# Optimization experiments

Hardware: AMD Instinct MI355X
Metric: run time of the kernel (lower is better)

Reference implementation:

```python
import jax, jax.numpy as jnp
import numpy as np

B, S, D = 1, 2048, 512
H, KH, DH = 8, 2, 64
G = H // KH            # grouped queries per kv head
CBS = SBS = 32         # compress / selection block size (equal)
NSEL = 8               # num selected blocks
WIN = 128              # sliding window size
NC = S // CBS          # num compressed blocks
NF = S // SBS          # num fine blocks (S divisible by SBS)
CDIM = CBS * DH


def setup_inputs():
    key = jax.random.key(0)
    ks = jax.random.split(key, 12)
    r = lambda k, shape, s=0.02: jax.random.normal(k, shape, dtype=jnp.float32) * s
    return {
        "inp": jax.random.normal(ks[0], (B, S, D), dtype=jnp.float32),
        "norm_w": jnp.ones((D,), jnp.float32),
        "w_qkv": r(ks[1], (D, H * DH + 2 * KH * DH)),
        "mem_kv": r(ks[2], (2, KH, 1, DH)),
        "k_pos": r(ks[3], (KH, CBS, DH)),
        "v_pos": r(ks[4], (KH, CBS, DH)),
        "kc_w1": r(ks[5], (CDIM, CDIM)), "kc_b1": jnp.zeros((CDIM,), jnp.float32),
        "kc_w2": r(ks[6], (CDIM, DH)), "kc_b2": jnp.zeros((DH,), jnp.float32),
        "vc_w1": r(ks[7], (CDIM, CDIM)), "vc_b1": jnp.zeros((CDIM,), jnp.float32),
        "vc_w2": r(ks[8], (CDIM, DH)), "vc_b2": jnp.zeros((DH,), jnp.float32),
        "comb_w": r(ks[9], (D, 3 * H)),
        "comb_b": jnp.tile(jnp.array([-2.0, -2.0, 2.0], jnp.float32), H),
        "out_w": r(ks[10], (H * DH, D)),
    }


def _rope(x):  # x: [b, h, n, d]; interleaved rotary (rotary-embedding-torch style)
    d, n = x.shape[-1], x.shape[-2]
    inv = 1.0 / (10000.0 ** (jnp.arange(0, d, 2, dtype=jnp.float32) / d))
    fr = jnp.arange(n, dtype=jnp.float32)[:, None] * inv[None, :]  # [n, d/2]
    fr = jnp.repeat(fr, 2, axis=-1)                                 # [n, d]
    cos, sin = jnp.cos(fr), jnp.sin(fr)
    xp = x.reshape(*x.shape[:-1], d // 2, 2)
    xr = jnp.stack((-xp[..., 1], xp[..., 0]), axis=-1).reshape(x.shape)
    return x * cos + xr * sin


def _mlp(x, w1, b1, w2, b2):
    return jax.nn.relu(x @ w1 + b1) @ w2 + b2


def _forward(inp, norm_w, w_qkv, mem_kv, k_pos, v_pos, kc_w1, kc_b1, kc_w2, kc_b2,
             vc_w1, vc_b1, vc_w2, vc_b2, comb_w, comb_b, out_w):
    scale = DH ** -0.5
    NEG = -jnp.finfo(jnp.float32).max

    # RMSNorm
    x = inp * jax.lax.rsqrt(jnp.mean(inp * inp, -1, keepdims=True)
                            + jnp.finfo(jnp.float32).eps) * norm_w

    qkv = x @ w_qkv
    q, k, v = jnp.split(qkv, [H * DH, H * DH + KH * DH], axis=-1)
    q = q.reshape(B, S, H, DH).transpose(0, 2, 1, 3)    # b h n d
    k = k.reshape(B, S, KH, DH).transpose(0, 2, 1, 3)   # b kh n d
    v = v.reshape(B, S, KH, DH).transpose(0, 2, 1, 3)

    # --- 1. compressed attention (unrotated q/k) ---
    kb = k.reshape(B, KH, NC, CBS, DH) + k_pos[None, :, None]
    vb = v.reshape(B, KH, NC, CBS, DH) + v_pos[None, :, None]
    ck = _mlp(kb.reshape(B, KH, NC, CDIM), kc_w1, kc_b1, kc_w2, kc_b2)  # b kh nc d
    cv = _mlp(vb.reshape(B, KH, NC, CDIM), vc_w1, vc_b1, vc_w2, vc_b2)
    ck = jnp.concatenate((jnp.broadcast_to(mem_kv[0][None], (B, KH, 1, DH)), ck), axis=2)
    cv = jnp.concatenate((jnp.broadcast_to(mem_kv[1][None], (B, KH, 1, DH)), cv), axis=2)

    ck_pos = jnp.concatenate((jnp.array([-1]), (jnp.arange(NC) + 1) * CBS - 1))
    cmask = ck_pos[None, :] < jnp.arange(S)[:, None]     # [S, 1+NC]

    qg = q.reshape(B, KH, G, S, DH)
    csim = jnp.einsum('bhgid,bhjd->bhgij', qg, ck) * scale
    csim = jnp.where(cmask, csim, NEG)
    cattn = jax.nn.softmax(csim, axis=-1)
    c_out = jnp.einsum('bhgij,bhjd->bhgid', cattn, cv)   # b kh g n d

    # --- importance scores -> top-k block selection (shared across grouped queries) ---
    imp = csim[..., 1:].mean(axis=2)                     # b kh n nc
    imp = jnp.pad(imp, ((0, 0), (0, 0), (0, 0), (1, 0)), constant_values=-1e3)
    imp = jax.nn.softmax(imp, axis=-1)[..., 1:]
    sel_val, sel_idx = jax.lax.top_k(imp, NSEL)          # b kh n sel

    # --- rotary for fine + sliding branches ---
    qr, kr = _rope(q), _rope(k)

    # --- 2. fine (selected-block) attention ---
    own = jnp.broadcast_to((jnp.arange(S) // SBS)[None, None, :, None], (B, KH, S, 1))
    sel_idx = jnp.concatenate((sel_idx, own), axis=-1)   # b kh n (sel+1), own block appended

    bmask = jnp.broadcast_to((sel_val > 1e-10)[..., None], (B, KH, S, NSEL, SBS))
    tri = jnp.tril(jnp.ones((SBS, SBS), bool))
    diag = jnp.broadcast_to(jnp.tile(tri, (NF, 1))[None, None, :, None, :], (B, KH, S, 1, SBS))
    fmask = jnp.concatenate((bmask, diag), axis=-2).reshape(B, KH, 1, S, (NSEL + 1) * SBS)

    kfb = kr.reshape(B, KH, NF, SBS, DH)
    vfb = v.reshape(B, KH, NF, SBS, DH)
    gidx = sel_idx[..., None, None]                      # b kh n sel1 1 1
    fk = jnp.take_along_axis(kfb[:, :, None], gidx, axis=3).reshape(B, KH, S, (NSEL + 1) * SBS, DH)
    fv = jnp.take_along_axis(vfb[:, :, None], gidx, axis=3).reshape(B, KH, S, (NSEL + 1) * SBS, DH)

    fqg = qr.reshape(B, KH, G, S, DH)
    fsim = jnp.einsum('bhgid,bhijd->bhgij', fqg, fk) * scale
    fsim = jnp.where(fmask, fsim, NEG)
    fattn = jax.nn.softmax(fsim, axis=-1)
    f_out = jnp.einsum('bhgij,bhijd->bhgid', fattn, fv)  # b kh g n d

    diff = jnp.arange(S)[:, None] - jnp.arange(S)[None, :]
    smask = (diff >= 0) & (diff <= WIN)
    ssim = jnp.einsum('bhgid,bhjd->bhgij', fqg, kr) * scale
    ssim = jnp.where(smask, ssim, NEG)
    sattn = jax.nn.softmax(ssim, axis=-1)
    s_out = jnp.einsum('bhgij,bhjd->bhgid', sattn, v)    # b kh g n d

    # --- learned gating combine over [compressed, fine, sliding] ---
    gates = jax.nn.sigmoid(x @ comb_w + comb_b).reshape(B, S, H, 3)
    gates = gates.transpose(0, 2, 1, 3).reshape(B, KH, G, S, 3)
    out = gates[..., 0:1] * c_out + gates[..., 1:2] * f_out + gates[..., 2:3] * s_out
    out = out.reshape(B, H, S, DH).transpose(0, 2, 1, 3).reshape(B, S, H * DH)
    return out @ out_w


def reference(inp, norm_w, w_qkv, mem_kv, k_pos, v_pos, kc_w1, kc_b1, kc_w2, kc_b2,
              vc_w1, vc_b1, vc_w2, vc_b2, comb_w, comb_b, out_w):
    return _forward(inp, norm_w, w_qkv, mem_kv, k_pos, v_pos, kc_w1, kc_b1, kc_w2, kc_b2,
                    vc_w1, vc_b1, vc_w2, vc_b2, comb_w, comb_b, out_w)
```

## Files before the change

kernel.cpp:

```cpp
#include <hip/hip_runtime.h>
#include <hip/hip_bf16.h>
#include <math.h>

#define S 2048
#define D 512
#define H 8
#define KH 2
#define DH 64
#define G 4
#define CBS 32
#define NSEL 8
#define WIN 128
#define NC 64
#define CDIM 2048

typedef __attribute__((ext_vector_type(8))) short bf16x8_t;
typedef __attribute__((ext_vector_type(4))) float f32x4_t;
typedef __attribute__((ext_vector_type(2))) _Float16 half2v;

static __device__ __forceinline__ unsigned short f2bf(float f) {
    union { float f; unsigned int u; } v; v.f = f;
    unsigned int r = (v.u + 0x7FFFu + ((v.u >> 16) & 1u)) >> 16;
    return (unsigned short)r;
}
static __device__ __forceinline__ float bf2f(unsigned short h) {
    union { unsigned int u; float f; } v; v.u = ((unsigned int)h) << 16;
    return v.f;
}
static __device__ __forceinline__ float bflo(unsigned int u) {
    union { unsigned int u; float f; } v; v.u = u << 16; return v.f;
}
static __device__ __forceinline__ float bfhi(unsigned int u) {
    union { unsigned int u; float f; } v; v.u = u & 0xffff0000u; return v.f;
}
static __device__ __forceinline__ unsigned short f2h(float f) {
    union { _Float16 h; unsigned short s; } v; v.h = (_Float16)f; return v.s;
}
static __device__ __forceinline__ float h2f(unsigned short u) {
    union { unsigned short s; _Float16 h; } v; v.s = u; return (float)v.h;
}
static __device__ __forceinline__ float dot2f16(unsigned int a, unsigned int b, float c) {
    union { unsigned int u; half2v h; } A, B; A.u = a; B.u = b;
    return __builtin_amdgcn_fdot2(A.h, B.h, c, false);
}

__global__ __launch_bounds__(256) void k_rmsnorm(const float* __restrict__ inp,
                                                 const float* __restrict__ w,
                                                 unsigned short* __restrict__ xbf) {
    int s = blockIdx.x; int t = threadIdx.x;
    const float* row = inp + (size_t)s * D;
    float a = row[t], b = row[t + 256];
    float ss = a * a + b * b;
    for (int off = 32; off; off >>= 1) ss += __shfl_xor(ss, off);
    __shared__ float red[4];
    if ((t & 63) == 0) red[t >> 6] = ss;
    __syncthreads();
    float tot = red[0] + red[1] + red[2] + red[3];
    float inv = rsqrtf(tot / (float)D + 1.1920929e-07f);
    xbf[(size_t)s * D + t]       = f2bf(a * inv * w[t]);
    xbf[(size_t)s * D + t + 256] = f2bf(b * inv * w[t + 256]);
}

__global__ void k_rope_table(float* __restrict__ ct, float* __restrict__ st) {
    int idx = blockIdx.x * 256 + threadIdx.x;
    int s = idx >> 5, p = idx & 31;
    float inv = powf(10000.0f, -(float)p / 32.0f);
    float fr = (float)s * inv;
    ct[idx] = cosf(fr); st[idx] = sinf(fr);
}

__global__ __launch_bounds__(256) void k_gemm0(
    const unsigned short* __restrict__ A,
    const float* __restrict__ W,
    const float* __restrict__ k_pos, const float* __restrict__ v_pos,
    const float* __restrict__ ct, const float* __restrict__ st,
    float* __restrict__ qb,
    unsigned short* __restrict__ qr16, unsigned short* __restrict__ kr16,
    unsigned short* __restrict__ v16, unsigned short* __restrict__ kbvb)
{
    const int K = 512, N = 768;
    __shared__ __align__(16) unsigned short As[64][40];
    __shared__ __align__(16) unsigned short Bs[64][40];
    int t = threadIdx.x;
    int m0 = blockIdx.y * 64, n0 = blockIdx.x * 64;
    int wave = t >> 6, lane = t & 63;
    int mh = wave & 1, nh = wave >> 1;
    f32x4_t acc[2][2] = {};
    int ar = t >> 2, ac = (t & 3) * 8;
    int bk = t >> 3, bn = (t & 7) * 8;
    int arow_l = lane & 15, kcol = (lane >> 4) * 8;
    uint4 aReg = *(const uint4*)&A[(size_t)(m0 + ar) * K + ac];
    const float4* wr = (const float4*)&W[(size_t)bk * N + n0 + bn];
    float4 w0 = wr[0], w1 = wr[1];
    for (int k0 = 0; k0 < K; k0 += 32) {
        __syncthreads();
        *(uint4*)&As[ar][ac] = aReg;
        unsigned short bp[8];
        bp[0] = f2bf(w0.x); bp[1] = f2bf(w0.y); bp[2] = f2bf(w0.z); bp[3] = f2bf(w0.w);
        bp[4] = f2bf(w1.x); bp[5] = f2bf(w1.y); bp[6] = f2bf(w1.z); bp[7] = f2bf(w1.w);
        #pragma unroll
        for (int j = 0; j < 8; ++j) Bs[bn + j][bk] = bp[j];
        __syncthreads();
        if (k0 + 32 < K) {
            aReg = *(const uint4*)&A[(size_t)(m0 + ar) * K + k0 + 32 + ac];
            wr = (const float4*)&W[(size_t)(k0 + 32 + bk) * N + n0 + bn];
            w0 = wr[0]; w1 = wr[1];
        }
        bf16x8_t a0 = *(const bf16x8_t*)&As[mh * 32 + arow_l][kcol];
        bf16x8_t a1 = *(const bf16x8_t*)&As[mh * 32 + 16 + arow_l][kcol];
        bf16x8_t b0v = *(const bf16x8_t*)&Bs[nh * 32 + arow_l][kcol];
        bf16x8_t b1v = *(const bf16x8_t*)&Bs[nh * 32 + 16 + arow_l][kcol];
        acc[0][0] = __builtin_amdgcn_mfma_f32_16x16x32_bf16(a0, b0v, acc[0][0], 0, 0, 0);
        acc[0][1] = __builtin_amdgcn_mfma_f32_16x16x32_bf16(a0, b1v, acc[0][1], 0, 0, 0);
        acc[1][0] = __builtin_amdgcn_mfma_f32_16x16x32_bf16(a1, b0v, acc[1][0], 0, 0, 0);
        acc[1][1] = __builtin_amdgcn_mfma_f32_16x16x32_bf16(a1, b1v, acc[1][1], 0, 0, 0);
    }
    #pragma unroll
    for (int mi = 0; mi < 2; ++mi)
    #pragma unroll
    for (int ni = 0; ni < 2; ++ni)
    #pragma unroll
    for (int r = 0; r < 4; ++r) {
        int gm = m0 + mh * 32 + mi * 16 + (lane >> 4) * 4 + r;
        int gn = n0 + nh * 32 + ni * 16 + (lane & 15);
        float val = acc[mi][ni][r];
        float part = __shfl_xor(val, 1);
        if (gn < 512) {
            int hh = gn >> 6, d = gn & 63;
            size_t idx = ((size_t)hh * S + gm) * DH + d;
            qb[idx] = val;
            int p = d >> 1;
            float cc = ct[gm * 32 + p], sn = st[gm * 32 + p];
            float y = (d & 1) ? (val * cc + part * sn) : (val * cc - part * sn);
            qr16[idx] = f2h(y);
        } else if (gn < 640) {
            int gk = gn - 512, khh = gk >> 6, d = gk & 63;
            size_t idx = ((size_t)khh * S + gm) * DH + d;
            int p = d >> 1;
            float cc = ct[gm * 32 + p], sn = st[gm * 32 + p];
            float y = (d & 1) ? (val * cc + part * sn) : (val * cc - part * sn);
            kr16[idx] = f2h(y);
            int tt = gm & 31, nc2 = gm >> 5;
            kbvb[((size_t)(khh * 64 + nc2)) * 2048 + tt * 64 + d] =
                f2bf(val + k_pos[(khh * CBS + tt) * 64 + d]);
        } else {
            int gv = gn - 640, khh = gv >> 6, d = gv & 63;
            size_t idx = ((size_t)khh * S + gm) * DH + d;
            v16[idx] = f2bf(val);
            int tt = gm & 31, nc2 = gm >> 5;
            kbvb[((size_t)(128 + khh * 64 + nc2)) * 2048 + tt * 64 + d] =
                f2bf(val + v_pos[(khh * CBS + tt) * 64 + d]);
        }
    }
}

template<int MODE>
__global__ __launch_bounds__(256) void k_gemm(
    const unsigned short* __restrict__ A,
    const float* __restrict__ B0,
    const float* __restrict__ B1,
    const float* __restrict__ bias0, const float* __restrict__ bias1,
    int M, int N, int K,
    unsigned short* __restrict__ hid, float* __restrict__ outC)
{
    __shared__ __align__(16) unsigned short As[64][40];
    __shared__ __align__(16) unsigned short Bs[64][40];
    int t = threadIdx.x;
    int m0 = blockIdx.y * 64, n0 = blockIdx.x * 64;
    const float* W = B0;
    const float* bias = bias0;
    if (MODE == 1 && blockIdx.y >= 2) { W = B1; bias = bias1; }
    int wave = t >> 6, lane = t & 63;
    int mh = wave & 1, nh = wave >> 1;
    f32x4_t acc[2][2] = {};
    int ar = t >> 2, ac = (t & 3) * 8;
    int bk = t >> 3, bn = (t & 7) * 8;
    int arow_l = lane & 15, kcol = (lane >> 4) * 8;
    uint4 aReg = *(const uint4*)&A[(size_t)(m0 + ar) * K + ac];
    const float4* wr = (const float4*)&W[(size_t)bk * N + n0 + bn];
    float4 w0 = wr[0], w1 = wr[1];
    for (int k0 = 0; k0 < K; k0 += 32) {
        __syncthreads();
        *(uint4*)&As[ar][ac] = aReg;
        unsigned short bp[8];
        bp[0] = f2bf(w0.x); bp[1] = f2bf(w0.y); bp[2] = f2bf(w0.z); bp[3] = f2bf(w0.w);
        bp[4] = f2bf(w1.x); bp[5] = f2bf(w1.y); bp[6] = f2bf(w1.z); bp[7] = f2bf(w1.w);
        #pragma unroll
        for (int j = 0; j < 8; ++j) Bs[bn + j][bk] = bp[j];
        __syncthreads();
        if (k0 + 32 < K) {
            aReg = *(const uint4*)&A[(size_t)(m0 + ar) * K + k0 + 32 + ac];
            wr = (const float4*)&W[(size_t)(k0 + 32 + bk) * N + n0 + bn];
            w0 = wr[0]; w1 = wr[1];
        }
        bf16x8_t a0 = *(const bf16x8_t*)&As[mh * 32 + arow_l][kcol];
        bf16x8_t a1 = *(const bf16x8_t*)&As[mh * 32 + 16 + arow_l][kcol];
        bf16x8_t b0v = *(const bf16x8_t*)&Bs[nh * 32 + arow_l][kcol];
        bf16x8_t b1v = *(const bf16x8_t*)&Bs[nh * 32 + 16 + arow_l][kcol];
        acc[0][0] = __builtin_amdgcn_mfma_f32_16x16x32_bf16(a0, b0v, acc[0][0], 0, 0, 0);
        acc[0][1] = __builtin_amdgcn_mfma_f32_16x16x32_bf16(a0, b1v, acc[0][1], 0, 0, 0);
        acc[1][0] = __builtin_amdgcn_mfma_f32_16x16x32_bf16(a1, b0v, acc[1][0], 0, 0, 0);
        acc[1][1] = __builtin_amdgcn_mfma_f32_16x16x32_bf16(a1, b1v, acc[1][1], 0, 0, 0);
    }
    #pragma unroll
    for (int mi = 0; mi < 2; ++mi)
    #pragma unroll
    for (int ni = 0; ni < 2; ++ni)
    #pragma unroll
    for (int r = 0; r < 4; ++r) {
        int gm = m0 + mh * 32 + mi * 16 + (lane >> 4) * 4 + r;
        int gn = n0 + nh * 32 + ni * 16 + (lane & 15);
        float val = acc[mi][ni][r];
        if (MODE == 1) {
            float h = val + bias[gn]; if (h < 0.f) h = 0.f;
            hid[(size_t)gm * N + gn] = f2bf(h);
        } else {
            outC[(size_t)gm * N + gn] = val;
        }
    }
}

__global__ __launch_bounds__(256) void k_mlp2p(
    const unsigned short* __restrict__ A,
    const float* __restrict__ kc_w2, const float* __restrict__ vc_w2,
    float* __restrict__ part)
{
    const int N = 64, LDA = 2048;
    __shared__ __align__(16) unsigned short As[64][40];
    __shared__ __align__(16) unsigned short Bs[64][40];
    int t = threadIdx.x;
    int ks = blockIdx.x, m0 = blockIdx.y * 64;
    int kbeg = ks * 512;
    const float* W = (blockIdx.y >= 2) ? vc_w2 : kc_w2;
    int wave = t >> 6, lane = t & 63;
    int mh = wave & 1, nh = wave >> 1;
    f32x4_t acc[2][2] = {};
    int ar = t >> 2, ac = (t & 3) * 8;
    int bk = t >> 3, bn = (t & 7) * 8;
    int arow_l = lane & 15, kcol = (lane >> 4) * 8;
    uint4 aReg = *(const uint4*)&A[(size_t)(m0 + ar) * LDA + kbeg + ac];
    const float4* wr = (const float4*)&W[(size_t)(kbeg + bk) * N + bn];
    float4 w0 = wr[0], w1 = wr[1];
    for (int k0 = 0; k0 < 512; k0 += 32) {
        __syncthreads();
        *(uint4*)&As[ar][ac] = aReg;
        unsigned short bp[8];
        bp[0] = f2bf(w0.x); bp[1] = f2bf(w0.y); bp[2] = f2bf(w0.z); bp[3] = f2bf(w0.w);
        bp[4] = f2bf(w1.x); bp[5] = f2bf(w1.y); bp[6] = f2bf(w1.z); bp[7] = f2bf(w1.w);
        #pragma unroll
        for (int j = 0; j < 8; ++j) Bs[bn + j][bk] = bp[j];
        __syncthreads();
        if (k0 + 32 < 512) {
            aReg = *(const uint4*)&A[(size_t)(m0 + ar) * LDA + kbeg + k0 + 32 + ac];
            wr = (const float4*)&W[(size_t)(kbeg + k0 + 32 + bk) * N + bn];
            w0 = wr[0]; w1 = wr[1];
        }
        bf16x8_t a0 = *(const bf16x8_t*)&As[mh * 32 + arow_l][kcol];
        bf16x8_t a1 = *(const bf16x8_t*)&As[mh * 32 + 16 + arow_l][kcol];
        bf16x8_t b0v = *(const bf16x8_t*)&Bs[nh * 32 + arow_l][kcol];
        bf16x8_t b1v = *(const bf16x8_t*)&Bs[nh * 32 + 16 + arow_l][kcol];
        acc[0][0] = __builtin_amdgcn_mfma_f32_16x16x32_bf16(a0, b0v, acc[0][0], 0, 0, 0);
        acc[0][1] = __builtin_amdgcn_mfma_f32_16x16x32_bf16(a0, b1v, acc[0][1], 0, 0, 0);
        acc[1][0] = __builtin_amdgcn_mfma_f32_16x16x32_bf16(a1, b0v, acc[1][0], 0, 0, 0);
        acc[1][1] = __builtin_amdgcn_mfma_f32_16x16x32_bf16(a1, b1v, acc[1][1], 0, 0, 0);
    }
    #pragma unroll
    for (int mi = 0; mi < 2; ++mi)
    #pragma unroll
    for (int ni = 0; ni < 2; ++ni)
    #pragma unroll
    for (int r = 0; r < 4; ++r) {
        int gm = m0 + mh * 32 + mi * 16 + (lane >> 4) * 4 + r;
        int gn = nh * 32 + ni * 16 + (lane & 15);
        part[((size_t)ks * 256 + gm) * 64 + gn] = acc[mi][ni][r];
    }
}

__global__ __launch_bounds__(256) void k_mlp2r(
    const float* __restrict__ part, const float* __restrict__ kc_b2,
    const float* __restrict__ vc_b2, const float* __restrict__ mem_kv,
    float* __restrict__ ck, float* __restrict__ cv)
{
    int idx = blockIdx.x * 256 + threadIdx.x;
    int gm = idx >> 6, gn = idx & 63;
    float sum = part[(size_t)gm * 64 + gn] + part[(size_t)(256 + gm) * 64 + gn]
              + part[(size_t)(512 + gm) * 64 + gn] + part[(size_t)(768 + gm) * 64 + gn];
    bool isv = gm >= 128;
    sum += isv ? vc_b2[gn] : kc_b2[gn];
    float* dst = isv ? cv : ck;
    int kh2 = (gm >> 6) & 1, nc2 = gm & 63;
    dst[(kh2 * 65 + 1 + nc2) * 64 + gn] = sum;
    if (blockIdx.x == 0 && threadIdx.x < 256) {
        int t = threadIdx.x;
        int path2 = t >> 7, khm = (t >> 6) & 1, dm = t & 63;
        float* dstm = path2 ? cv : ck;
        dstm[khm * 65 * 64 + dm] = mem_kv[path2 * (KH * DH) + khm * DH + dm];
    }
}

__global__ __launch_bounds__(256) void k_cattn(
    const float* __restrict__ q, const float* __restrict__ ck, const float* __restrict__ cv,
    float* __restrict__ c_out, int* __restrict__ sel)
{
    int kh = blockIdx.x >> 9, sc = blockIdx.x & 511;
    int s_base = sc * 4;
    __shared__ float ckT[64][65];
    __shared__ float cvL[64][66];
    __shared__ float qL[4][64];
    __shared__ float simL[4][64];
    __shared__ float pL[4][64];
    int t = threadIdx.x;
    for (int idx = t; idx < 4096; idx += 256) {
        int j = idx >> 6, d = idx & 63;
        ckT[d][j] = ck[(kh * 65 + j) * 64 + d];
        cvL[j][d] = cv[(kh * 65 + j) * 64 + d];
    }
    int g = t >> 6, lane = t & 63;
    for (int si = 0; si < 4; ++si) {
        int s = s_base + si;
        __syncthreads();
        qL[g][lane] = q[((kh * G + g) * S + s) * DH + lane];
        __syncthreads();
        int j = lane;
        bool valid = (j == 0) || (s >= j * 32);
        float sim = 0.f;
        #pragma unroll 8
        for (int d = 0; d < 64; ++d) sim += qL[g][d] * ckT[d][j];
        sim *= 0.125f;
        float simm = valid ? sim : -INFINITY;
        simL[g][j] = simm;
        float m = simm;
        for (int off = 32; off; off >>= 1) m = fmaxf(m, __shfl_xor(m, off));
        float p = valid ? __expf(simm - m) : 0.f;
        float den = p;
        for (int off = 32; off; off >>= 1) den += __shfl_xor(den, off);
        pL[g][j] = p / den;
        float acc = 0.f;
        #pragma unroll
        for (int j4 = 0; j4 < 16; ++j4) {
            float4 p4 = *(const float4*)&pL[g][j4 * 4];
            acc += p4.x * cvL[j4 * 4 + 0][lane] + p4.y * cvL[j4 * 4 + 1][lane]
                 + p4.z * cvL[j4 * 4 + 2][lane] + p4.w * cvL[j4 * 4 + 3][lane];
        }
        c_out[((kh * G + g) * S + s) * DH + lane] = acc;
        __syncthreads();
        if (g == 0) {
            int l = lane;
            float lv = -INFINITY;
            if (l < 63 && s >= (l + 1) * 32)
                lv = 0.25f * (simL[0][l + 1] + simL[1][l + 1] + simL[2][l + 1] + simL[3][l + 1]);
            float mm = lv;
            for (int off = 32; off; off >>= 1) mm = fmaxf(mm, __shfl_xor(mm, off));
            mm = fmaxf(mm, -1000.0f);
            float e = (lv == -INFINITY) ? 0.f : __expf(lv - mm);
            float dd = e;
            for (int off = 32; off; off >>= 1) dd += __shfl_xor(dd, off);
            dd += __expf(-1000.0f - mm);
            float val = e / dd;
            float vc = val;
            int base = (kh * S + s) * 9;
            for (int t8 = 0; t8 < 8; ++t8) {
                float bv2 = vc; int bi = l;
                for (int off = 32; off; off >>= 1) {
                    float ov = __shfl_xor(bv2, off); int oi = __shfl_xor(bi, off);
                    if (ov > bv2 || (ov == bv2 && oi < bi)) { bv2 = ov; bi = oi; }
                }
                if (l == 0) sel[base + t8] = (bv2 > 1e-10f) ? bi : -1;
                if (l == bi) vc = -1.f;
            }
            if (l == 0) sel[base + 8] = s >> 5;
        }
    }
}

__global__ __launch_bounds__(256, 4) void k_swattn(
    const unsigned short* __restrict__ qr16, const unsigned short* __restrict__ kr16,
    const unsigned short* __restrict__ v16, const int* __restrict__ sel,
    float* __restrict__ fob, float* __restrict__ sob)
{
    int kh = blockIdx.x >> 11, s = blockIdx.x & 2047;
    int t = threadIdx.x, w = t >> 6, lane = t & 63, g = w;
    __shared__ __align__(16) unsigned char KL[64 * 128];
    __shared__ __align__(16) unsigned char VL[64 * 144];
    __shared__ unsigned short qL16[4][64];
    __shared__ float pL[4][64];

    qL16[g][lane] = qr16[(((size_t)kh * G + g) * S + s) * DH + lane];

    int own_t = s & 31;
    int base = (kh * S + s) * 9;
    int lo = s - WIN; if (lo < 0) lo = 0;

    int nv = 0;
    #pragma unroll
    for (int i = 0; i < 8; ++i) nv += (sel[base + i] >= 0) ? 1 : 0;
    int npairF = (nv + 1) >> 1;
    int nchF = npairF + 1;
    int nchS = (s - lo + 63) >> 6;
    int nch = nchF + nchS;

    float lF = 0.f, a0F = 0.f, a1F = 0.f;
    float lS = 0.f, a0S = 0.f, a1S = 0.f;
    int h = lane >> 5, dhalf = lane & 31;
    int key = w * 16 + (lane & 15);
    int grpA = lane >> 4;
    uint4 z = make_uint4(0, 0, 0, 0);
    uint4 kd0 = z, kd1 = z, vd0 = z, vd1 = z;

    auto issue = [&](int c) {
        int gkey; bool kv;
        if (c < npairF) {
            int b = sel[base + 2 * c + ((key >> 5) & 1)];
            kv = b >= 0;
            gkey = (kv ? b : 0) * 32 + (key & 31);
        } else if (c == npairF) {
            kv = key < 32;
            gkey = (s & ~31) + (key & 31);
        } else {
            gkey = lo + (c - nchF) * 64 + key;
            kv = gkey < s;
        }
        const uint4* kp = (const uint4*)&kr16[((size_t)kh * S + gkey) * DH];
        const uint4* vp = (const uint4*)&v16 [((size_t)kh * S + gkey) * DH];
        kd0 = kv ? kp[grpA] : z;
        kd1 = kv ? kp[grpA + 4] : z;
        vd0 = kv ? vp[grpA] : z;
        vd1 = kv ? vp[grpA + 4] : z;
    };

    issue(0);
    for (int c = 0; c < nch; ++c) {
        __syncthreads();
        *(uint4*)(KL + key * 128 + 16 * (grpA ^ (key & 7))) = kd0;
        *(uint4*)(KL + key * 128 + 16 * ((grpA + 4) ^ (key & 7))) = kd1;
        *(uint4*)(VL + key * 144 + 16 * grpA) = vd0;
        *(uint4*)(VL + key * 144 + 16 * (grpA + 4)) = vd1;
        __syncthreads();
        if (c + 1 < nch) issue(c + 1);

        int j = lane;
        bool valid;
        if (c < npairF)       valid = (j < 32) || ((2 * c + 1) < nv);
        else if (c == npairF) valid = (j < 32) && (j <= own_t);
        else                  valid = (lo + (c - nchF) * 64 + j) < s;

        float sva = 0.f, svb = 0.f, svc = 0.f, svd = 0.f;
        #pragma unroll
        for (int grp = 0; grp < 8; ++grp) {
            uint4 kk = *(const uint4*)(KL + j * 128 + 16 * (grp ^ (j & 7)));
            uint4 qq = *(const uint4*)((const unsigned char*)qL16 + g * 128 + 16 * grp);
            sva = dot2f16(kk.x, qq.x, sva);
            svb = dot2f16(kk.y, qq.y, svb);
            svc = dot2f16(kk.z, qq.z, svc);
            svd = dot2f16(kk.w, qq.w, svd);
        }
        float sv = (sva + svb) + (svc + svd);
        float p = valid ? __expf(sv * 0.125f) : 0.f;
        float ps = p;
        for (int off = 32; off; off >>= 1) ps += __shfl_xor(ps, off);
        pL[g][j] = p;
        float t0 = 0.f, t1 = 0.f;
        #pragma unroll
        for (int j4 = 0; j4 < 8; ++j4) {
            float4 p4 = *(const float4*)&pL[g][h * 32 + j4 * 4];
            const float* pp = (const float*)&p4;
            #pragma unroll
            for (int qq = 0; qq < 4; ++qq) {
                unsigned int v2 = *(const unsigned int*)(VL + (h * 32 + j4 * 4 + qq) * 144 + 4 * dhalf);
                t0 += pp[qq] * bflo(v2);
                t1 += pp[qq] * bfhi(v2);
            }
        }
        if (c < nchF) { lF += ps; a0F += t0; a1F += t1; }
        else          { lS += ps; a0S += t0; a1S += t1; }
    }
    {
        float pr = h2f(qL16[g][lane]) * h2f(kr16[((size_t)kh * S + s) * DH + lane]);
        for (int off = 32; off; off >>= 1) pr += __shfl_xor(pr, off);
        float p = __expf(pr * 0.125f);
        lS += p;
        if (h == 0) {
            unsigned int v2 = *(const unsigned int*)&v16[(((size_t)kh * S + s) * DH) + 2 * dhalf];
            a0S += p * bflo(v2);
            a1S += p * bfhi(v2);
        }
    }
    a0F += __shfl_xor(a0F, 32);
    a1F += __shfl_xor(a1F, 32);
    a0S += __shfl_xor(a0S, 32);
    a1S += __shfl_xor(a1S, 32);
    if (lane < 32) {
        size_t ob = (((size_t)kh * G + g) * S + s) * DH + 2 * dhalf;
        float invF = 1.f / lF, invS = 1.f / lS;
        *(float2*)&fob[ob] = make_float2(a0F * invF, a1F * invF);
        *(float2*)&sob[ob] = make_float2(a0S * invS, a1S * invS);
    }
}

__global__ __launch_bounds__(256) void k_combine(
    const unsigned short* __restrict__ xbf, const float* __restrict__ comb_w, const float* __restrict__ comb_b,
    const float* __restrict__ c_out, const float* __restrict__ f_out, const float* __restrict__ s_out,
    unsigned short* __restrict__ comb)
{
    int s = blockIdx.x, t = threadIdx.x;
    __shared__ float gpart[24][8];
    __shared__ float gates[24];
    if (t < 192) {
        int cc = t >> 3, pt = t & 7;
        float sum = 0.f;
        for (int d = pt * 64; d < pt * 64 + 64; ++d)
            sum += bf2f(xbf[s * D + d]) * comb_w[d * 24 + cc];
        gpart[cc][pt] = sum;
    }
    __syncthreads();
    if (t < 24) {
        float sum = comb_b[t];
        for (int i = 0; i < 8; ++i) sum += gpart[t][i];
        gates[t] = 1.f / (1.f + __expf(-sum));
    }
    __syncthreads();
    for (int o = t; o < 512; o += 256) {
        int h = o >> 6, d = o & 63;
        int idx = (h * S + s) * DH + d;
        float r = gates[h * 3] * c_out[idx] + gates[h * 3 + 1] * f_out[idx] + gates[h * 3 + 2] * s_out[idx];
        comb[s * D + o] = f2bf(r);
    }
}

extern "C" void kernel_launch(void* const* d_in, const int* in_sizes, int n_in,
                              void* d_out, int out_size, void* d_ws, size_t ws_size,
                              hipStream_t stream)
{
    (void)in_sizes; (void)n_in; (void)out_size; (void)ws_size;
    const float* inp    = (const float*)d_in[0];
    const float* norm_w = (const float*)d_in[1];
    const float* w_qkv  = (const float*)d_in[2];
    const float* mem_kv = (const float*)d_in[3];
    const float* k_pos  = (const float*)d_in[4];
    const float* v_pos  = (const float*)d_in[5];
    const float* kc_w1  = (const float*)d_in[6];
    const float* kc_b1  = (const float*)d_in[7];
    const float* kc_w2  = (const float*)d_in[8];
    const float* kc_b2  = (const float*)d_in[9];
    const float* vc_w1  = (const float*)d_in[10];
    const float* vc_b1  = (const float*)d_in[11];
    const float* vc_w2  = (const float*)d_in[12];
    const float* vc_b2  = (const float*)d_in[13];
    const float* comb_w = (const float*)d_in[14];
    const float* comb_b = (const float*)d_in[15];
    const float* out_w  = (const float*)d_in[16];
    float* out = (float*)d_out;

    char* w = (char*)d_ws;
    size_t off = 0;
    auto alloc = [&](size_t bytes) { void* p = w + off; off += (bytes + 255) & ~(size_t)255; return p; };
    unsigned short* xbf   = (unsigned short*)alloc((size_t)S * D * 2);
    unsigned short* kbvb  = (unsigned short*)alloc((size_t)256 * 2048 * 2);
    unsigned short* hid   = (unsigned short*)alloc((size_t)256 * 2048 * 2);
    unsigned short* combb = (unsigned short*)alloc((size_t)S * 512 * 2);
    unsigned short* qr16  = (unsigned short*)alloc((size_t)H * S * DH * 2);
    unsigned short* kr16  = (unsigned short*)alloc((size_t)KH * S * DH * 2);
    unsigned short* v16   = (unsigned short*)alloc((size_t)KH * S * DH * 2);
    float* qb   = (float*)alloc((size_t)H * S * DH * 4);
    float* ckb  = (float*)alloc((size_t)KH * 65 * 64 * 4);
    float* cvb  = (float*)alloc((size_t)KH * 65 * 64 * 4);
    float* cob  = (float*)alloc((size_t)H * S * DH * 4);
    float* fob  = (float*)alloc((size_t)H * S * DH * 4);
    float* sob  = (float*)alloc((size_t)H * S * DH * 4);
    float* ctab = (float*)alloc((size_t)S * 32 * 4);
    float* stab = (float*)alloc((size_t)S * 32 * 4);
    float* partb = (float*)alloc((size_t)4 * 256 * 64 * 4);
    int*   selb = (int*)alloc((size_t)KH * S * 9 * 4);

    k_rope_table<<<(S * 32) / 256, 256, 0, stream>>>(ctab, stab);

    k_rmsnorm<<<S, 256, 0, stream>>>(inp, norm_w, xbf);

    k_gemm0<<<dim3(768 / 64, S / 64), 256, 0, stream>>>(
        xbf, w_qkv, k_pos, v_pos, ctab, stab, qb, qr16, kr16, v16, kbvb);

    k_gemm<1><<<dim3(2048 / 64, 256 / 64), 256, 0, stream>>>(
        kbvb, kc_w1, vc_w1, kc_b1, vc_b1, 256, 2048, 2048,
        hid, nullptr);

    k_mlp2p<<<dim3(4, 4), 256, 0, stream>>>(hid, kc_w2, vc_w2, partb);
    k_mlp2r<<<64, 256, 0, stream>>>(partb, kc_b2, vc_b2, mem_kv, ckb, cvb);

    k_cattn<<<KH * 512, 256, 0, stream>>>(qb, ckb, cvb, cob, selb);

    k_swattn<<<KH * S, 256, 0, stream>>>(qr16, kr16, v16, selb, fob, sob);

    k_combine<<<S, 256, 0, stream>>>(xbf, comb_w, comb_b, cob, fob, sob, combb);
    k_gemm<2><<<dim3(512 / 64, S / 64), 256, 0, stream>>>(
        combb, out_w, nullptr, nullptr, nullptr, S, 512, 512,
        nullptr, out);
}
```

Baseline: 248.2 us.

## Split-K the compression MLP first GEMM and merge own-block chunk into window

The first compression-MLP GEMM is split along K into two halves, which doubles the grid from 128 to 256 blocks; a separate reduction kernel then sums the partials, adds the bias, applies ReLU and converts to bf16. In the sliding/fine attention kernel, the dedicated chunk that loaded the query's own fine block is removed. Its keys are instead taken from the last sliding-window chunk, using prefix/suffix masking to feed both accumulators. The row-sum reductions are also deferred to a single shuffle at the end. This trades an extra launch and fp32 partial traffic for better GPU occupancy, and saves one load/compute chunk per query.

```diff
diff --git a/kernel.cpp b/kernel.cpp
--- a/kernel.cpp
+++ b/kernel.cpp
@@ -158,18 +158,14 @@
 __global__ __launch_bounds__(256) void k_gemm(
     const unsigned short* __restrict__ A,
     const float* __restrict__ B0,
-    const float* __restrict__ B1,
-    const float* __restrict__ bias0, const float* __restrict__ bias1,
     int M, int N, int K,
-    unsigned short* __restrict__ hid, float* __restrict__ outC)
+    float* __restrict__ outC)
 {
     __shared__ __align__(16) unsigned short As[64][40];
     __shared__ __align__(16) unsigned short Bs[64][40];
     int t = threadIdx.x;
     int m0 = blockIdx.y * 64, n0 = blockIdx.x * 64;
     const float* W = B0;
-    const float* bias = bias0;
-    if (MODE == 1 && blockIdx.y >= 2) { W = B1; bias = bias1; }
     int wave = t >> 6, lane = t & 63;
     int mh = wave & 1, nh = wave >> 1;
     f32x4_t acc[2][2] = {};
@@ -210,14 +206,82 @@
     for (int r = 0; r < 4; ++r) {
         int gm = m0 + mh * 32 + mi * 16 + (lane >> 4) * 4 + r;
         int gn = n0 + nh * 32 + ni * 16 + (lane & 15);
-        float val = acc[mi][ni][r];
-        if (MODE == 1) {
-            float h = val + bias[gn]; if (h < 0.f) h = 0.f;
-            hid[(size_t)gm * N + gn] = f2bf(h);
-        } else {
-            outC[(size_t)gm * N + gn] = val;
-        }
-    }
+        outC[(size_t)gm * N + gn] = acc[mi][ni][r];
+    }
+}
+
+__global__ __launch_bounds__(256) void k_gemm1p(
+    const unsigned short* __restrict__ A,
+    const float* __restrict__ kc_w1, const float* __restrict__ vc_w1,
+    float* __restrict__ part)
+{
+    const int N = 2048, LDA = 2048;
+    __shared__ __align__(16) unsigned short As[64][40];
+    __shared__ __align__(16) unsigned short Bs[64][40];
+    int t = threadIdx.x;
+    int mb = blockIdx.y & 3, ks = blockIdx.y >> 2;
+    int m0 = mb * 64, n0 = blockIdx.x * 64, kbeg = ks * 1024;
+    const float* W = (mb >= 2) ? vc_w1 : kc_w1;
+    int wave = t >> 6, lane = t & 63;
+    int mh = wave & 1, nh = wave >> 1;
+    f32x4_t acc[2][2] = {};
+    int ar = t >> 2, ac = (t & 3) * 8;
+    int bk = t >> 3, bn = (t & 7) * 8;
+    int arow_l = lane & 15, kcol = (lane >> 4) * 8;
+    uint4 aReg = *(const uint4*)&A[(size_t)(m0 + ar) * LDA + kbeg + ac];
+    const float4* wr = (const float4*)&W[(size_t)(kbeg + bk) * N + n0 + bn];
+    float4 w0 = wr[0], w1 = wr[1];
+    for (int k0 = 0; k0 < 1024; k0 += 32) {
+        __syncthreads();
+        *(uint4*)&As[ar][ac] = aReg;
+        unsigned short bp[8];
+        bp[0] = f2bf(w0.x); bp[1] = f2bf(w0.y); bp[2] = f2bf(w0.z); bp[3] = f2bf(w0.w);
+        bp[4] = f2bf(w1.x); bp[5] = f2bf(w1.y); bp[6] = f2bf(w1.z); bp[7] = f2bf(w1.w);
+        #pragma unroll
+        for (int j = 0; j < 8; ++j) Bs[bn + j][bk] = bp[j];
+        __syncthreads();
+        if (k0 + 32 < 1024) {
+            aReg = *(const uint4*)&A[(size_t)(m0 + ar) * LDA + kbeg + k0 + 32 + ac];
+            wr = (const float4*)&W[(size_t)(kbeg + k0 + 32 + bk) * N + n0 + bn];
+            w0 = wr[0]; w1 = wr[1];
+        }
+        bf16x8_t a0 = *(const bf16x8_t*)&As[mh * 32 + arow_l][kcol];
+        bf16x8_t a1 = *(const bf16x8_t*)&As[mh * 32 + 16 + arow_l][kcol];
+        bf16x8_t b0v = *(const bf16x8_t*)&Bs[nh * 32 + arow_l][kcol];
+        bf16x8_t b1v = *(const bf16x8_t*)&Bs[nh * 32 + 16 + arow_l][kcol];
+        acc[0][0] = __builtin_amdgcn_mfma_f32_16x16x32_bf16(a0, b0v, acc[0][0], 0, 0, 0);
+        acc[0][1] = __builtin_amdgcn_mfma_f32_16x16x32_bf16(a0, b1v, acc[0][1], 0, 0, 0);
+        acc[1][0] = __builtin_amdgcn_mfma_f32_16x16x32_bf16(a1, b0v, acc[1][0], 0, 0, 0);
+        acc[1][1] = __builtin_amdgcn_mfma_f32_16x16x32_bf16(a1, b1v, acc[1][1], 0, 0, 0);
+    }
+    #pragma unroll
+    for (int mi = 0; mi < 2; ++mi)
+    #pragma unroll
+    for (int ni = 0; ni < 2; ++ni)
+    #pragma unroll
+    for (int r = 0; r < 4; ++r) {
+        int gm = m0 + mh * 32 + mi * 16 + (lane >> 4) * 4 + r;
+        int gn = n0 + nh * 32 + ni * 16 + (lane & 15);
+        part[((size_t)ks * 256 + gm) * N + gn] = acc[mi][ni][r];
+    }
+}
+
+__global__ __launch_bounds__(256) void k_gemm1r(
+    const float4* __restrict__ part, const float* __restrict__ kc_b1,
+    const float* __restrict__ vc_b1, uint2* __restrict__ hid)
+{
+    int idx = blockIdx.x * 256 + threadIdx.x;
+    int gm = idx >> 9, gn4 = (idx & 511) * 4;
+    float4 a = part[idx], b = part[idx + 131072];
+    const float* bias = (gm >= 128) ? vc_b1 : kc_b1;
+    float r0 = fmaxf(a.x + b.x + bias[gn4 + 0], 0.f);
+    float r1 = fmaxf(a.y + b.y + bias[gn4 + 1], 0.f);
+    float r2 = fmaxf(a.z + b.z + bias[gn4 + 2], 0.f);
+    float r3 = fmaxf(a.w + b.w + bias[gn4 + 3], 0.f);
+    uint2 o;
+    o.x = (unsigned)f2bf(r0) | ((unsigned)f2bf(r1) << 16);
+    o.y = (unsigned)f2bf(r2) | ((unsigned)f2bf(r3) << 16);
+    hid[idx] = o;
 }
 
 __global__ __launch_bounds__(256) void k_mlp2p(
@@ -387,7 +451,6 @@
 
     qL16[g][lane] = qr16[(((size_t)kh * G + g) * S + s) * DH + lane];
 
-    int own_t = s & 31;
     int base = (kh * S + s) * 9;
     int lo = s - WIN; if (lo < 0) lo = 0;
 
@@ -395,12 +458,13 @@
     #pragma unroll
     for (int i = 0; i < 8; ++i) nv += (sel[base + i] >= 0) ? 1 : 0;
     int npairF = (nv + 1) >> 1;
-    int nchF = npairF + 1;
     int nchS = (s - lo + 63) >> 6;
-    int nch = nchF + nchS;
-
-    float lF = 0.f, a0F = 0.f, a1F = 0.f;
-    float lS = 0.f, a0S = 0.f, a1S = 0.f;
+    int nch = npairF + nchS;
+    int ownStart = s & ~31;
+    bool hasOwn = (s & 31) != 0;
+
+    float lF = 0.f, lS = 0.f;
+    float a0F = 0.f, a1F = 0.f, a0S = 0.f, a1S = 0.f;
     int h = lane >> 5, dhalf = lane & 31;
     int key = w * 16 + (lane & 15);
     int grpA = lane >> 4;
@@ -413,11 +477,8 @@
             int b = sel[base + 2 * c + ((key >> 5) & 1)];
             kv = b >= 0;
             gkey = (kv ? b : 0) * 32 + (key & 31);
-        } else if (c == npairF) {
-            kv = key < 32;
-            gkey = (s & ~31) + (key & 31);
         } else {
-            gkey = lo + (c - nchF) * 64 + key;
+            gkey = lo + (c - npairF) * 64 + key;
             kv = gkey < s;
         }
         const uint4* kp = (const uint4*)&kr16[((size_t)kh * S + gkey) * DH];
@@ -439,10 +500,11 @@
         if (c + 1 < nch) issue(c + 1);
 
         int j = lane;
-        bool valid;
-        if (c < npairF)       valid = (j < 32) || ((2 * c + 1) < nv);
-        else if (c == npairF) valid = (j < 32) && (j <= own_t);
-        else                  valid = (lo + (c - nchF) * 64 + j) < s;
+        bool isPair = c < npairF;
+        int cs = c - npairF;
+        int gk0 = lo + cs * 64;
+        bool valid = isPair ? ((j < 32) || ((2 * c + 1) < nv))
+                            : ((gk0 + j) < s);
 
         float sva = 0.f, svb = 0.f, svc = 0.f, svd = 0.f;
         #pragma unroll
@@ -456,33 +518,65 @@
         }
         float sv = (sva + svb) + (svc + svd);
         float p = valid ? __expf(sv * 0.125f) : 0.f;
-        float ps = p;
-        for (int off = 32; off; off >>= 1) ps += __shfl_xor(ps, off);
         pL[g][j] = p;
-        float t0 = 0.f, t1 = 0.f;
-        #pragma unroll
-        for (int j4 = 0; j4 < 8; ++j4) {
-            float4 p4 = *(const float4*)&pL[g][h * 32 + j4 * 4];
-            const float* pp = (const float*)&p4;
+
+        bool doOwn = (!isPair) && hasOwn && (cs == nchS - 1);
+        if (!doOwn) {
+            if (isPair) lF += p; else lS += p;
+            float t0 = 0.f, t1 = 0.f;
             #pragma unroll
-            for (int qq = 0; qq < 4; ++qq) {
-                unsigned int v2 = *(const unsigned int*)(VL + (h * 32 + j4 * 4 + qq) * 144 + 4 * dhalf);
-                t0 += pp[qq] * bflo(v2);
-                t1 += pp[qq] * bfhi(v2);
+            for (int j4 = 0; j4 < 8; ++j4) {
+                float4 p4 = *(const float4*)&pL[g][h * 32 + j4 * 4];
+                const float* pp = (const float*)&p4;
+                #pragma unroll
+                for (int q2 = 0; q2 < 4; ++q2) {
+                    unsigned int v2 = *(const unsigned int*)(VL + (h * 32 + j4 * 4 + q2) * 144 + 4 * dhalf);
+                    t0 += pp[q2] * bflo(v2);
+                    t1 += pp[q2] * bfhi(v2);
+                }
             }
-        }
-        if (c < nchF) { lF += ps; a0F += t0; a1F += t1; }
-        else          { lS += ps; a0S += t0; a1S += t1; }
+            if (isPair) { a0F += t0; a1F += t1; }
+            else        { a0S += t0; a1S += t1; }
+        } else {
+            lS += p;
+            int jstart = ownStart - gk0;
+            if (j >= jstart) lF += p;
+            float pre0 = 0.f, pre1 = 0.f, suf0 = 0.f, suf1 = 0.f;
+            #pragma unroll
+            for (int j4 = 0; j4 < 8; ++j4) {
+                float4 p4 = *(const float4*)&pL[g][h * 32 + j4 * 4];
+                const float* pp = (const float*)&p4;
+                #pragma unroll
+                for (int q2 = 0; q2 < 4; ++q2) {
+                    int jj = h * 32 + j4 * 4 + q2;
+                    unsigned int v2 = *(const unsigned int*)(VL + jj * 144 + 4 * dhalf);
+                    float t0 = pp[q2] * bflo(v2);
+                    float t1 = pp[q2] * bfhi(v2);
+                    bool inSuf = jj >= jstart;
+                    suf0 += inSuf ? t0 : 0.f;
+                    suf1 += inSuf ? t1 : 0.f;
+                    pre0 += inSuf ? 0.f : t0;
+                    pre1 += inSuf ? 0.f : t1;
+                }
+            }
+            a0S += pre0 + suf0; a1S += pre1 + suf1;
+            a0F += suf0;        a1F += suf1;
+        }
     }
     {
         float pr = h2f(qL16[g][lane]) * h2f(kr16[((size_t)kh * S + s) * DH + lane]);
         for (int off = 32; off; off >>= 1) pr += __shfl_xor(pr, off);
-        float p = __expf(pr * 0.125f);
-        lS += p;
+        float pd = __expf(pr * 0.125f);
+        for (int off = 32; off; off >>= 1) {
+            lF += __shfl_xor(lF, off);
+            lS += __shfl_xor(lS, off);
+        }
+        lF += pd; lS += pd;
         if (h == 0) {
             unsigned int v2 = *(const unsigned int*)&v16[(((size_t)kh * S + s) * DH) + 2 * dhalf];
-            a0S += p * bflo(v2);
-            a1S += p * bfhi(v2);
+            float b0 = bflo(v2), b1 = bfhi(v2);
+            a0F += pd * b0; a1F += pd * b1;
+            a0S += pd * b0; a1S += pd * b1;
         }
     }
     a0F += __shfl_xor(a0F, 32);
@@ -570,6 +664,7 @@
     float* ctab = (float*)alloc((size_t)S * 32 * 4);
     float* stab = (float*)alloc((size_t)S * 32 * 4);
     float* partb = (float*)alloc((size_t)4 * 256 * 64 * 4);
+    float* g1part = (float*)alloc((size_t)2 * 256 * 2048 * 4);
     int*   selb = (int*)alloc((size_t)KH * S * 9 * 4);
 
     k_rope_table<<<(S * 32) / 256, 256, 0, stream>>>(ctab, stab);
@@ -579,9 +674,8 @@
     k_gemm0<<<dim3(768 / 64, S / 64), 256, 0, stream>>>(
         xbf, w_qkv, k_pos, v_pos, ctab, stab, qb, qr16, kr16, v16, kbvb);
 
-    k_gemm<1><<<dim3(2048 / 64, 256 / 64), 256, 0, stream>>>(
-        kbvb, kc_w1, vc_w1, kc_b1, vc_b1, 256, 2048, 2048,
-        hid, nullptr);
+    k_gemm1p<<<dim3(32, 8), 256, 0, stream>>>(kbvb, kc_w1, vc_w1, g1part);
+    k_gemm1r<<<512, 256, 0, stream>>>((const float4*)g1part, kc_b1, vc_b1, (uint2*)hid);
 
     k_mlp2p<<<dim3(4, 4), 256, 0, stream>>>(hid, kc_w2, vc_w2, partb);
     k_mlp2r<<<64, 256, 0, stream>>>(partb, kc_b2, vc_b2, mem_kv, ckb, cvb);
@@ -592,6 +686,5 @@
 
     k_combine<<<S, 256, 0, stream>>>(xbf, comb_w, comb_b, cob, fob, sob, combb);
     k_gemm<2><<<dim3(512 / 64, S / 64), 256, 0, stream>>>(
-        combb, out_w, nullptr, nullptr, nullptr, S, 512, 512,
-        nullptr, out);
-}
+        combb, out_w, S, 512, 512, out);
+}
```

Result: faster. 220.2 us (-11.3%).
